# Performance work log

Hardware: AMD Instinct MI355X
Metric: run time of the kernel (lower is better)

The kernel has to match this reference:

```python
import jax, jax.numpy as jnp
import numpy as np

B, T, D = 16, 512, 256
HS, D_A, R = 512, 64, 8


def setup_inputs() -> dict:
    key = jax.random.key(0)
    ks = jax.random.split(key, 8)
    s = lambda *sh: 1.0 / np.sqrt(sh[0])
    x = jax.random.normal(ks[0], (B, T, D), dtype=jnp.float32)
    w_first = jax.random.normal(ks[1], (D, D_A), dtype=jnp.float32) * s(D)
    b_first = jnp.zeros((D_A,), dtype=jnp.float32)
    w_second = jax.random.normal(ks[2], (D_A, R), dtype=jnp.float32) * s(D_A)
    b_second = jnp.zeros((R,), dtype=jnp.float32)
    weight_iBarh = jax.random.normal(ks[3], (D, 4 * HS), dtype=jnp.float32) * s(D)
    weight_hh = jax.random.normal(ks[4], (HS, 4 * HS), dtype=jnp.float32) * s(HS)
    bias = jnp.zeros((4 * HS,), dtype=jnp.float32)
    return {"x": x, "w_first": w_first, "b_first": b_first,
            "w_second": w_second, "b_second": b_second,
            "weight_iBarh": weight_iBarh, "weight_hh": weight_hh, "bias": bias}


def _forward(x, w_first, b_first, w_second, b_second, weight_iBarh, weight_hh, bias):
    b, t, d = x.shape
    hs = weight_hh.shape[0]
    r = w_second.shape[1]
    # attention logits for every timestep: (B, T, r)
    s = jnp.tanh(x @ w_first + b_first) @ w_second + b_second
    # causal mask: query t attends to keys j <= t
    mask = jnp.tril(jnp.ones((t, t), dtype=bool))  # (t_query, j_key)
    # logits: (B, Tq, Tk, r); softmax over key axis per (t, r), masked to prefix
    logits = jnp.where(mask[None, :, :, None], s[:, None, :, :], -jnp.inf)
    attn = jax.nn.softmax(logits, axis=2).mean(axis=-1)  # (B, Tq, Tk) == mean over r
    # M_t = attention-weighted average of prefix inputs: (B, T, D)
    M = jnp.einsum('btj,bjd->btd', attn, x)
    gates_x = jnp.einsum('btd,dg->btg', M, weight_iBarh) + bias  # (B, T, 4H)

    def step(carry, gx):
        h, c = carry
        g = gx + h @ weight_hh  # (B, 4H)
        i = jax.nn.sigmoid(g[:, :hs])
        f = jax.nn.sigmoid(g[:, hs:2 * hs])
        gg = jnp.tanh(g[:, 2 * hs:3 * hs])
        o = jax.nn.sigmoid(g[:, 3 * hs:])
        c = f * c + i * gg
        h = o * jnp.tanh(c)
        return (h, c), h

    h0 = jnp.zeros((b, hs), dtype=x.dtype)
    c0 = jnp.zeros((b, hs), dtype=x.dtype)
    (h_t, c_t), hseq = jax.lax.scan(step, (h0, c0), jnp.swapaxes(gates_x, 0, 1))
    hidden_seq = jnp.swapaxes(hseq, 0, 1)  # (B, T, H)
    return hidden_seq, h_t, c_t


def reference(x, w_first, b_first, w_second, b_second, weight_iBarh, weight_hh, bias):
    return _forward(x, w_first, b_first, w_second, b_second, weight_iBarh, weight_hh, bias)
```

## Files before the change

kernel.cpp:

```cpp
#include <hip/hip_runtime.h>
#include <math.h>

#define BB 16
#define TT 512
#define DD 256
#define HS 512
#define DA 64
#define RR 8
#define G4H 2048

typedef __attribute__((ext_vector_type(2))) float f2;


__global__ __launch_bounds__(256) void k1_score(
    const float* __restrict__ x, const float* __restrict__ w1,
    const float* __restrict__ b1, const float* __restrict__ w2,
    const float* __restrict__ b2, float* __restrict__ s_out) {
  const int wave = threadIdx.x >> 6;
  const int lane = threadIdx.x & 63;
  for (int i = 0; i < 4; ++i) {
    const int bt = blockIdx.x * 16 + wave * 4 + i;
    const float* xr = x + bt * DD;
    float acc = b1[lane];
    #pragma unroll 4
    for (int d = 0; d < DD; ++d)
      acc = fmaf(xr[d], w1[d * DA + lane], acc);
    const float a = tanhf(acc);
    #pragma unroll
    for (int r = 0; r < RR; ++r) {
      float v = a * w2[lane * RR + r];
      for (int off = 32; off > 0; off >>= 1) v += __shfl_xor(v, off);
      if (lane == 0) s_out[bt * RR + r] = v + b2[r];
    }
  }
}

__global__ __launch_bounds__(512) void k2_prefix(
    const float* __restrict__ s_in, float* __restrict__ e_out,
    float* __restrict__ inv_out) {
  const int b = blockIdx.x >> 3, r = blockIdx.x & 7;
  const int t = threadIdx.x;
  __shared__ float red[TT];
  __shared__ float buf[2][TT];
  const float v = s_in[(b * TT + t) * RR + r];
  red[t] = v;
  __syncthreads();
  for (int off = 256; off >= 1; off >>= 1) {
    if (t < off) red[t] = fmaxf(red[t], red[t + off]);
    __syncthreads();
  }
  const float m = red[0];
  const float e = expf(v - m);
  int p = 0;
  buf[0][t] = e;
  __syncthreads();
  for (int off = 1; off < TT; off <<= 1) {
    const float add = (t >= off) ? buf[p][t - off] : 0.f;
    buf[1 - p][t] = buf[p][t] + add;
    __syncthreads();
    p ^= 1;
  }
  const float den = buf[p][t];
  e_out[(b * TT + t) * RR + r] = e;
  inv_out[(b * TT + t) * RR + r] = 1.0f / den;
}

__global__ __launch_bounds__(64) void k3_mix(
    const float* __restrict__ x, const float* __restrict__ e_in,
    const float* __restrict__ inv_in, float* __restrict__ Mout) {
  const int b = blockIdx.x >> 2;
  const int d = (blockIdx.x & 3) * 64 + threadIdx.x;
  __shared__ __align__(16) float el[TT * RR];
  __shared__ __align__(16) float il[TT * RR];
  for (int i = threadIdx.x * 4; i < TT * RR; i += 64 * 4) {
    *(float4*)&el[i] = *(const float4*)&e_in[b * TT * RR + i];
    *(float4*)&il[i] = *(const float4*)&inv_in[b * TT * RR + i];
  }
  __syncthreads();
  float4 c0 = {0.f, 0.f, 0.f, 0.f}, c1 = {0.f, 0.f, 0.f, 0.f};
  for (int t = 0; t < TT; ++t) {
    const float xv = x[(b * TT + t) * DD + d];
    const float4 e0 = *(const float4*)&el[t * RR];
    const float4 e1 = *(const float4*)&el[t * RR + 4];
    const float4 i0 = *(const float4*)&il[t * RR];
    const float4 i1 = *(const float4*)&il[t * RR + 4];
    c0.x = fmaf(e0.x, xv, c0.x); c0.y = fmaf(e0.y, xv, c0.y);
    c0.z = fmaf(e0.z, xv, c0.z); c0.w = fmaf(e0.w, xv, c0.w);
    c1.x = fmaf(e1.x, xv, c1.x); c1.y = fmaf(e1.y, xv, c1.y);
    c1.z = fmaf(e1.z, xv, c1.z); c1.w = fmaf(e1.w, xv, c1.w);
    float msum = c0.x * i0.x + c0.y * i0.y + c0.z * i0.z + c0.w * i0.w;
    msum += c1.x * i1.x + c1.y * i1.y + c1.z * i1.z + c1.w * i1.w;
    Mout[(b * TT + t) * DD + d] = msum * 0.125f;
  }
}

__global__ __launch_bounds__(256) void k4_gemm(
    const float* __restrict__ A, const float* __restrict__ Bw,
    const float* __restrict__ bias, float* __restrict__ C) {
  const int bn = blockIdx.x & 15;
  const int bm = blockIdx.x >> 4;
  const int tid = threadIdx.x;
  const int tx = tid & 15, ty = tid >> 4;
  __shared__ __align__(16) float As[16][132];
  __shared__ __align__(16) float Bs[16][132];
  const int row0 = bm * 128, col0 = bn * 128;

  float acc[2][4][2][4];
  #pragma unroll
  for (int a = 0; a < 2; ++a)
    #pragma unroll
    for (int i = 0; i < 4; ++i)
      #pragma unroll
      for (int q = 0; q < 2; ++q)
        #pragma unroll
        for (int j = 0; j < 4; ++j) acc[a][i][q][j] = 0.f;

  const int arow = tid >> 1, akc = (tid & 1) * 8;
  const int bkr = tid >> 4, bcc = (tid & 15) * 8;

  for (int k0 = 0; k0 < 256; k0 += 16) {
    const float4 a0 = *(const float4*)&A[(row0 + arow) * 256 + k0 + akc];
    const float4 a1 = *(const float4*)&A[(row0 + arow) * 256 + k0 + akc + 4];
    const float4 b0 = *(const float4*)&Bw[(k0 + bkr) * 2048 + col0 + bcc];
    const float4 b1 = *(const float4*)&Bw[(k0 + bkr) * 2048 + col0 + bcc + 4];
    __syncthreads();
    As[akc + 0][arow] = a0.x; As[akc + 1][arow] = a0.y;
    As[akc + 2][arow] = a0.z; As[akc + 3][arow] = a0.w;
    As[akc + 4][arow] = a1.x; As[akc + 5][arow] = a1.y;
    As[akc + 6][arow] = a1.z; As[akc + 7][arow] = a1.w;
    *(float4*)&Bs[bkr][bcc] = b0;
    *(float4*)&Bs[bkr][bcc + 4] = b1;
    __syncthreads();
    #pragma unroll
    for (int kk = 0; kk < 16; ++kk) {
      float av[8], bv[8];
      *(float4*)&av[0] = *(const float4*)&As[kk][ty * 4];
      *(float4*)&av[4] = *(const float4*)&As[kk][64 + ty * 4];
      *(float4*)&bv[0] = *(const float4*)&Bs[kk][tx * 4];
      *(float4*)&bv[4] = *(const float4*)&Bs[kk][64 + tx * 4];
      #pragma unroll
      for (int a = 0; a < 2; ++a)
        #pragma unroll
        for (int i = 0; i < 4; ++i)
          #pragma unroll
          for (int q = 0; q < 2; ++q)
            #pragma unroll
            for (int j = 0; j < 4; ++j)
              acc[a][i][q][j] = fmaf(av[a * 4 + i], bv[q * 4 + j], acc[a][i][q][j]);
    }
  }
  const float4 bias0 = *(const float4*)&bias[col0 + tx * 4];
  const float4 bias1 = *(const float4*)&bias[col0 + 64 + tx * 4];
  #pragma unroll
  for (int a = 0; a < 2; ++a)
    #pragma unroll
    for (int i = 0; i < 4; ++i) {
      const int row = row0 + a * 64 + ty * 4 + i;
      float4 v0, v1;
      v0.x = acc[a][i][0][0] + bias0.x; v0.y = acc[a][i][0][1] + bias0.y;
      v0.z = acc[a][i][0][2] + bias0.z; v0.w = acc[a][i][0][3] + bias0.w;
      v1.x = acc[a][i][1][0] + bias1.x; v1.y = acc[a][i][1][1] + bias1.y;
      v1.z = acc[a][i][1][2] + bias1.z; v1.w = acc[a][i][1][3] + bias1.w;
      *(float4*)&C[row * 2048 + col0 + tx * 4] = v0;
      *(float4*)&C[row * 2048 + col0 + 64 + tx * 4] = v1;
    }
}

__device__ __forceinline__ float fast_sigmoid(float x) {
  return __builtin_amdgcn_rcpf(1.f + __expf(-x));
}
__device__ __forceinline__ float fast_tanh(float x) {
  const float xc = fmaxf(x, -30.f);
  const float e = __expf(-2.f * xc);
  return (1.f - e) * __builtin_amdgcn_rcpf(1.f + e);
}

__device__ __forceinline__ unsigned long long poll_ld(
    const unsigned long long* p) {
  return __hip_atomic_load(p, __ATOMIC_RELAXED, __HIP_MEMORY_SCOPE_AGENT);
}

__global__ __launch_bounds__(512, 1) void k5_lstm(
    const float* __restrict__ gates, const float* __restrict__ whh,
    float* __restrict__ out, unsigned long long* hbuf) {
  const int s   = blockIdx.x & 15;
  const int b   = blockIdx.x >> 4;
  const int tid = threadIdx.x;
  const int kq  = tid & 15;
  const int cq  = tid >> 4;
  const int j0  = s * 32;
  const int unit = j0 + cq;

  __shared__ __align__(16) float Wl[256 * 128];
  __shared__ __align__(16) float hl[2][576];

  f2 wrA[32], wrB[32];
  for (int rnd = 0; rnd < 2; ++rnd) {
    for (int i = tid * 4; i < 256 * 128; i += 512 * 4) {
      const int k = i >> 7, c = i & 127;
      *(float4*)&Wl[i] =
          *(const float4*)&whh[(rnd * 256 + k) * G4H + (c >> 5) * HS + j0 + (c & 31)];
    }
    __syncthreads();
    if ((kq >> 3) == rnd) {
      const int kb = (kq & 7) * 32;
      #pragma unroll
      for (int kk = 0; kk < 32; ++kk) {
        const int base = (kb + kk) * 128 + cq;
        wrA[kk].x = *(volatile const float*)&Wl[base];
        wrA[kk].y = *(volatile const float*)&Wl[base + 32];
        wrB[kk].x = *(volatile const float*)&Wl[base + 64];
        wrB[kk].y = *(volatile const float*)&Wl[base + 96];
      }
    }
    __syncthreads();
  }

  float c_reg = 0.f;

  float4 g_cur = {0, 0, 0, 0}, g_n1 = {0, 0, 0, 0};
  const float* gbase = gates + (long)b * TT * G4H + unit;
  if (kq == 0) {
    g_cur.x = gbase[0];            g_cur.y = gbase[HS];
    g_cur.z = gbase[2 * HS];       g_cur.w = gbase[3 * HS];
    const float* g1 = gbase + G4H;
    g_n1.x = g1[0];                g_n1.y = g1[HS];
    g_n1.z = g1[2 * HS];           g_n1.w = g1[3 * HS];
  }

  for (int t = 0; t < TT; ++t) {
    const int par = t & 1;
    if (t > 0) {
      const unsigned long long* ha =
          hbuf + (((t - 1) & 1) * BB + b) * HS + tid;
      unsigned long long pkt;
      do {
        pkt = poll_ld(ha);
      } while ((unsigned)(pkt >> 32) < (unsigned)t);
      hl[par][(tid >> 5) * 36 + (tid & 31)] = __uint_as_float((unsigned)pkt);
    }
    float4 g_n2 = {0, 0, 0, 0};
    if (kq == 0) {
      const int tn = (t + 2 < TT) ? t + 2 : TT - 1;
      const float* g2 = gbase + (long)tn * G4H;
      g_n2.x = g2[0];        g_n2.y = g2[HS];
      g_n2.z = g2[2 * HS];   g_n2.w = g2[3 * HS];
    }
    __asm__ __volatile__("s_waitcnt lgkmcnt(0)\ns_barrier" ::: "memory");
    f2 acc01 = {0.f, 0.f}, acc23 = {0.f, 0.f};
    if (t > 0) {
      const float* hb = &hl[par][kq * 36];
      #pragma unroll
      for (int i = 0; i < 8; ++i) {
        const float4 h4 = *(const float4*)(hb + i * 4);
        const f2 hx = {h4.x, h4.x}, hy = {h4.y, h4.y};
        const f2 hz = {h4.z, h4.z}, hw = {h4.w, h4.w};
        acc01 += wrA[i * 4 + 0] * hx;  acc23 += wrB[i * 4 + 0] * hx;
        acc01 += wrA[i * 4 + 1] * hy;  acc23 += wrB[i * 4 + 1] * hy;
        acc01 += wrA[i * 4 + 2] * hz;  acc23 += wrB[i * 4 + 2] * hz;
        acc01 += wrA[i * 4 + 3] * hw;  acc23 += wrB[i * 4 + 3] * hw;
      }
    }
    #pragma unroll
    for (int off = 1; off <= 8; off <<= 1) {
      acc01.x += __shfl_xor(acc01.x, off);
      acc01.y += __shfl_xor(acc01.y, off);
      acc23.x += __shfl_xor(acc23.x, off);
      acc23.y += __shfl_xor(acc23.y, off);
    }
    if (kq == 0) {
      const float I = fast_sigmoid(acc01.x + g_cur.x);
      const float F = fast_sigmoid(acc01.y + g_cur.y);
      const float G = fast_tanh(acc23.x + g_cur.z);
      const float O = fast_sigmoid(acc23.y + g_cur.w);
      c_reg = F * c_reg + I * G;
      const float h = O * fast_tanh(c_reg);
      const unsigned long long pkt =
          ((unsigned long long)(unsigned)(t + 1) << 32) |
          (unsigned long long)__float_as_uint(h);
      __hip_atomic_store(&hbuf[(par * BB + b) * HS + unit], pkt,
                         __ATOMIC_RELAXED, __HIP_MEMORY_SCOPE_AGENT);
      out[((long)b * TT + t) * HS + unit] = h;
      if (t == TT - 1) {
        out[(long)BB * TT * HS + b * HS + unit] = h;
        out[(long)BB * TT * HS + BB * HS + b * HS + unit] = c_reg;
      }
    }
    g_cur = g_n1;
    g_n1 = g_n2;
  }
}

extern "C" void kernel_launch(void* const* d_in, const int* in_sizes, int n_in,
                              void* d_out, int out_size, void* d_ws,
                              size_t ws_size, hipStream_t stream) {
  const float* x    = (const float*)d_in[0];
  const float* w1   = (const float*)d_in[1];
  const float* b1   = (const float*)d_in[2];
  const float* w2   = (const float*)d_in[3];
  const float* b2   = (const float*)d_in[4];
  const float* wih  = (const float*)d_in[5];
  const float* whh  = (const float*)d_in[6];
  const float* bias = (const float*)d_in[7];
  float* out = (float*)d_out;

  float* ws = (float*)d_ws;
  float* s_buf  = ws;
  float* e_buf  = ws + 65536;
  float* i_buf  = ws + 131072;
  float* M_buf  = ws + 196608;
  float* g_buf  = ws + 2293760;
  unsigned long long* hbuf64 = (unsigned long long*)ws;

  k1_score<<<512, 256, 0, stream>>>(x, w1, b1, w2, b2, s_buf);
  k2_prefix<<<BB * RR, 512, 0, stream>>>(s_buf, e_buf, i_buf);
  k3_mix<<<64, 64, 0, stream>>>(x, e_buf, i_buf, M_buf);
  k4_gemm<<<64 * 16, 256, 0, stream>>>(M_buf, wih, bias, g_buf);
  hipMemsetAsync(hbuf64, 0, 2 * BB * HS * sizeof(unsigned long long), stream);
  k5_lstm<<<256, 512, 0, stream>>>(g_buf, whh, out, hbuf64);
}
```

Before: 1.162 ms.

## Use bf16 MFMA for input-gate GEMM and stagger LSTM h polling order

The input projection GEMM moves from an FP32 FMA tile kernel to bf16 MFMA 16x16x32 instructions. The mix kernel now writes M as bf16, and a new kernel transposes and converts W_ih to bf16 on every call. Separately, the LSTM kernel permutes which hidden unit each thread polls so that blocks do not all spin on the same addresses. This lowers GEMM precision to bf16 inputs and adds an extra transpose launch, but the GEMM is likely a small share of total time next to the sequential LSTM.

```diff
diff --git a/kernel.cpp b/kernel.cpp
--- a/kernel.cpp
+++ b/kernel.cpp
@@ -10,7 +10,30 @@
 #define G4H 2048
 
 typedef __attribute__((ext_vector_type(2))) float f2;
-
+typedef __attribute__((ext_vector_type(8))) short bf16x8;
+typedef __attribute__((ext_vector_type(4))) float f32x4;
+typedef unsigned short ushort_t;
+
+
+__device__ __forceinline__ ushort_t f2bf(float f) {
+  const unsigned u = __float_as_uint(f);
+  return (ushort_t)((u + 0x7FFFu + ((u >> 16) & 1u)) >> 16);
+}
+
+__global__ __launch_bounds__(256) void k0w_transpose(
+    const float* __restrict__ W, ushort_t* __restrict__ Wt) {
+  __shared__ float tl[64][65];
+  const int kb = (blockIdx.x & 3) * 64;
+  const int nb = (blockIdx.x >> 2) * 64;
+  const int tid = threadIdx.x;
+  for (int i = tid; i < 4096; i += 256)
+    tl[i >> 6][i & 63] = W[(kb + (i >> 6)) * 2048 + nb + (i & 63)];
+  __syncthreads();
+  for (int i = tid; i < 4096; i += 256) {
+    const int n = i >> 6, k = i & 63;
+    Wt[(nb + n) * 256 + kb + k] = f2bf(tl[k][n]);
+  }
+}
 
 __global__ __launch_bounds__(256) void k1_score(
     const float* __restrict__ x, const float* __restrict__ w1,
@@ -67,7 +90,7 @@
 
 __global__ __launch_bounds__(64) void k3_mix(
     const float* __restrict__ x, const float* __restrict__ e_in,
-    const float* __restrict__ inv_in, float* __restrict__ Mout) {
+    const float* __restrict__ inv_in, ushort_t* __restrict__ Mout) {
   const int b = blockIdx.x >> 2;
   const int d = (blockIdx.x & 3) * 64 + threadIdx.x;
   __shared__ __align__(16) float el[TT * RR];
@@ -90,80 +113,67 @@
     c1.z = fmaf(e1.z, xv, c1.z); c1.w = fmaf(e1.w, xv, c1.w);
     float msum = c0.x * i0.x + c0.y * i0.y + c0.z * i0.z + c0.w * i0.w;
     msum += c1.x * i1.x + c1.y * i1.y + c1.z * i1.z + c1.w * i1.w;
-    Mout[(b * TT + t) * DD + d] = msum * 0.125f;
-  }
-}
-
-__global__ __launch_bounds__(256) void k4_gemm(
-    const float* __restrict__ A, const float* __restrict__ Bw,
+    Mout[(b * TT + t) * DD + d] = f2bf(msum * 0.125f);
+  }
+}
+
+__global__ __launch_bounds__(256) void k4_mfma(
+    const ushort_t* __restrict__ Mb, const ushort_t* __restrict__ Wtb,
     const float* __restrict__ bias, float* __restrict__ C) {
   const int bn = blockIdx.x & 15;
   const int bm = blockIdx.x >> 4;
   const int tid = threadIdx.x;
-  const int tx = tid & 15, ty = tid >> 4;
-  __shared__ __align__(16) float As[16][132];
-  __shared__ __align__(16) float Bs[16][132];
+  const int wv = tid >> 6, lane = tid & 63;
+  const int quad = lane >> 4, l16 = lane & 15;
+  const int wm = (wv & 1) * 64, wn = (wv >> 1) * 64;
   const int row0 = bm * 128, col0 = bn * 128;
 
-  float acc[2][4][2][4];
+  __shared__ __align__(16) ushort_t As[128][40];
+  __shared__ __align__(16) ushort_t Bs[128][40];
+
+  f32x4 acc[4][4];
   #pragma unroll
-  for (int a = 0; a < 2; ++a)
-    #pragma unroll
-    for (int i = 0; i < 4; ++i)
+  for (int i = 0; i < 4; ++i)
+    #pragma unroll
+    for (int j = 0; j < 4; ++j) acc[i][j] = (f32x4){0.f, 0.f, 0.f, 0.f};
+
+  const int r = tid >> 1, koff = (tid & 1) * 16;
+  for (int k0 = 0; k0 < 256; k0 += 32) {
+    const uint4 av0 = *(const uint4*)&Mb[(row0 + r) * 256 + k0 + koff];
+    const uint4 av1 = *(const uint4*)&Mb[(row0 + r) * 256 + k0 + koff + 8];
+    const uint4 bv0 = *(const uint4*)&Wtb[(col0 + r) * 256 + k0 + koff];
+    const uint4 bv1 = *(const uint4*)&Wtb[(col0 + r) * 256 + k0 + koff + 8];
+    __syncthreads();
+    *(uint4*)&As[r][koff] = av0; *(uint4*)&As[r][koff + 8] = av1;
+    *(uint4*)&Bs[r][koff] = bv0; *(uint4*)&Bs[r][koff + 8] = bv1;
+    __syncthreads();
+    bf16x8 af[4], bfr[4];
+    #pragma unroll
+    for (int mi = 0; mi < 4; ++mi)
+      af[mi] = *(const bf16x8*)&As[wm + mi * 16 + l16][quad * 8];
+    #pragma unroll
+    for (int ni = 0; ni < 4; ++ni)
+      bfr[ni] = *(const bf16x8*)&Bs[wn + ni * 16 + l16][quad * 8];
+    #pragma unroll
+    for (int mi = 0; mi < 4; ++mi)
       #pragma unroll
-      for (int q = 0; q < 2; ++q)
-        #pragma unroll
-        for (int j = 0; j < 4; ++j) acc[a][i][q][j] = 0.f;
-
-  const int arow = tid >> 1, akc = (tid & 1) * 8;
-  const int bkr = tid >> 4, bcc = (tid & 15) * 8;
-
-  for (int k0 = 0; k0 < 256; k0 += 16) {
-    const float4 a0 = *(const float4*)&A[(row0 + arow) * 256 + k0 + akc];
-    const float4 a1 = *(const float4*)&A[(row0 + arow) * 256 + k0 + akc + 4];
-    const float4 b0 = *(const float4*)&Bw[(k0 + bkr) * 2048 + col0 + bcc];
-    const float4 b1 = *(const float4*)&Bw[(k0 + bkr) * 2048 + col0 + bcc + 4];
-    __syncthreads();
-    As[akc + 0][arow] = a0.x; As[akc + 1][arow] = a0.y;
-    As[akc + 2][arow] = a0.z; As[akc + 3][arow] = a0.w;
-    As[akc + 4][arow] = a1.x; As[akc + 5][arow] = a1.y;
-    As[akc + 6][arow] = a1.z; As[akc + 7][arow] = a1.w;
-    *(float4*)&Bs[bkr][bcc] = b0;
-    *(float4*)&Bs[bkr][bcc + 4] = b1;
-    __syncthreads();
-    #pragma unroll
-    for (int kk = 0; kk < 16; ++kk) {
-      float av[8], bv[8];
-      *(float4*)&av[0] = *(const float4*)&As[kk][ty * 4];
-      *(float4*)&av[4] = *(const float4*)&As[kk][64 + ty * 4];
-      *(float4*)&bv[0] = *(const float4*)&Bs[kk][tx * 4];
-      *(float4*)&bv[4] = *(const float4*)&Bs[kk][64 + tx * 4];
+      for (int ni = 0; ni < 4; ++ni)
+        acc[mi][ni] = __builtin_amdgcn_mfma_f32_16x16x32_bf16(
+            af[mi], bfr[ni], acc[mi][ni], 0, 0, 0);
+  }
+  #pragma unroll
+  for (int ni = 0; ni < 4; ++ni) {
+    const int col = col0 + wn + ni * 16 + l16;
+    const float bv = bias[col];
+    #pragma unroll
+    for (int mi = 0; mi < 4; ++mi) {
       #pragma unroll
-      for (int a = 0; a < 2; ++a)
-        #pragma unroll
-        for (int i = 0; i < 4; ++i)
-          #pragma unroll
-          for (int q = 0; q < 2; ++q)
-            #pragma unroll
-            for (int j = 0; j < 4; ++j)
-              acc[a][i][q][j] = fmaf(av[a * 4 + i], bv[q * 4 + j], acc[a][i][q][j]);
-    }
-  }
-  const float4 bias0 = *(const float4*)&bias[col0 + tx * 4];
-  const float4 bias1 = *(const float4*)&bias[col0 + 64 + tx * 4];
-  #pragma unroll
-  for (int a = 0; a < 2; ++a)
-    #pragma unroll
-    for (int i = 0; i < 4; ++i) {
-      const int row = row0 + a * 64 + ty * 4 + i;
-      float4 v0, v1;
-      v0.x = acc[a][i][0][0] + bias0.x; v0.y = acc[a][i][0][1] + bias0.y;
-      v0.z = acc[a][i][0][2] + bias0.z; v0.w = acc[a][i][0][3] + bias0.w;
-      v1.x = acc[a][i][1][0] + bias1.x; v1.y = acc[a][i][1][1] + bias1.y;
-      v1.z = acc[a][i][1][2] + bias1.z; v1.w = acc[a][i][1][3] + bias1.w;
-      *(float4*)&C[row * 2048 + col0 + tx * 4] = v0;
-      *(float4*)&C[row * 2048 + col0 + 64 + tx * 4] = v1;
-    }
+      for (int rg = 0; rg < 4; ++rg) {
+        const int row = row0 + wm + mi * 16 + quad * 4 + rg;
+        C[(long)row * 2048 + col] = acc[mi][ni][rg] + bv;
+      }
+    }
+  }
 }
 
 __device__ __forceinline__ float fast_sigmoid(float x) {
@@ -190,6 +200,8 @@
   const int cq  = tid >> 4;
   const int j0  = s * 32;
   const int unit = j0 + cq;
+  const int pu = (j0 + kq * 32 + cq) & 511;
+  const int puslot = (pu >> 5) * 36 + (pu & 31);
 
   __shared__ __align__(16) float Wl[256 * 128];
   __shared__ __align__(16) float hl[2][576];
@@ -232,12 +244,12 @@
     const int par = t & 1;
     if (t > 0) {
       const unsigned long long* ha =
-          hbuf + (((t - 1) & 1) * BB + b) * HS + tid;
+          hbuf + (((t - 1) & 1) * BB + b) * HS + pu;
       unsigned long long pkt;
       do {
         pkt = poll_ld(ha);
       } while ((unsigned)(pkt >> 32) < (unsigned)t);
-      hl[par][(tid >> 5) * 36 + (tid & 31)] = __uint_as_float((unsigned)pkt);
+      hl[par][puslot] = __uint_as_float((unsigned)pkt);
     }
     float4 g_n2 = {0, 0, 0, 0};
     if (kq == 0) {
@@ -308,14 +320,16 @@
   float* s_buf  = ws;
   float* e_buf  = ws + 65536;
   float* i_buf  = ws + 131072;
-  float* M_buf  = ws + 196608;
+  ushort_t* Mb  = (ushort_t*)(ws + 196608);
+  ushort_t* Wtb = (ushort_t*)(ws + 1245184);
   float* g_buf  = ws + 2293760;
   unsigned long long* hbuf64 = (unsigned long long*)ws;
 
+  k0w_transpose<<<128, 256, 0, stream>>>(wih, Wtb);
   k1_score<<<512, 256, 0, stream>>>(x, w1, b1, w2, b2, s_buf);
   k2_prefix<<<BB * RR, 512, 0, stream>>>(s_buf, e_buf, i_buf);
-  k3_mix<<<64, 64, 0, stream>>>(x, e_buf, i_buf, M_buf);
-  k4_gemm<<<64 * 16, 256, 0, stream>>>(M_buf, wih, bias, g_buf);
+  k3_mix<<<64, 64, 0, stream>>>(x, e_buf, i_buf, Mb);
+  k4_mfma<<<64 * 16, 256, 0, stream>>>(Mb, Wtb, bias, g_buf);
   hipMemsetAsync(hbuf64, 0, 2 * BB * HS * sizeof(unsigned long long), stream);
   k5_lstm<<<256, 512, 0, stream>>>(g_buf, whh, out, hbuf64);
 }
```

New measurement: 1.154 ms. Within noise of the previous version (-0.7%).
